# Optimization experiments

Measured on AMD Instinct MI355X. Metric: run time of the kernel, lower is better.

## Reference

```python
import jax, jax.numpy as jnp
import numpy as np

H_GRU = 32  # GRU hidden size fixed to 32 in the module


def setup_inputs() -> dict:
    key = jax.random.key(0)
    ks = jax.random.split(key, 12)
    B, C_in, H, W = 64, 64, 48, 160
    C_out = 64
    s_in = 1.0 / np.sqrt(C_in)
    s_h = 1.0 / np.sqrt(H_GRU)
    u = lambda k, shape: jax.random.uniform(k, shape, jnp.float32, -s_h, s_h)
    return {
        "x": jax.random.normal(ks[0], (B, C_in, H, W), jnp.float32),
        "conv_w": jax.random.normal(ks[1], (C_out, C_in), jnp.float32) * s_in,
        "conv_b": jax.random.normal(ks[2], (C_out,), jnp.float32) * s_in,
        "wih_f": u(ks[3], (3 * H_GRU, C_out)),
        "whh_f": u(ks[4], (3 * H_GRU, H_GRU)),
        "bih_f": u(ks[5], (3 * H_GRU,)),
        "bhh_f": u(ks[6], (3 * H_GRU,)),
        "wih_b": u(ks[7], (3 * H_GRU, C_out)),
        "whh_b": u(ks[8], (3 * H_GRU, H_GRU)),
        "bih_b": u(ks[9], (3 * H_GRU,)),
        "bhh_b": u(ks[10], (3 * H_GRU,)),
    }


def _gru_scan(pre, whh, bhh):
    # pre: [N, T, 3H] input-side gate pre-activations (already x@Wih^T + bih)
    N = pre.shape[0]

    def step(h, g):
        gh = h @ whh.T + bhh
        gi_r, gi_z, gi_n = jnp.split(g, 3, axis=-1)
        gh_r, gh_z, gh_n = jnp.split(gh, 3, axis=-1)
        r = jax.nn.sigmoid(gi_r + gh_r)
        z = jax.nn.sigmoid(gi_z + gh_z)
        n = jnp.tanh(gi_n + r * gh_n)
        h_new = (1.0 - z) * n + z * h
        return h_new, h_new

    h0 = jnp.zeros((N, H_GRU), pre.dtype)
    _, ys = jax.lax.scan(step, h0, jnp.swapaxes(pre, 0, 1))  # ys: [T, N, H]
    return jnp.swapaxes(ys, 0, 1)  # [N, T, H]


def reference(x, conv_w, conv_b, wih_f, whh_f, bih_f, bhh_f,
              wih_b, whh_b, bih_b, bhh_b):
    B, C_in, H, W = x.shape
    # 1x1 conv fused with the NCHW->NHWC permute
    y = jnp.einsum('bchw,oc->bhwo', x, conv_w) + conv_b  # [B, H, W, C_out]
    C_out = y.shape[-1]
    seq = y.reshape(B * H, W, C_out)  # GRU batch = B*H, seq_len = W
    # forward direction
    pre_f = jnp.einsum('ntc,gc->ntg', seq, wih_f) + bih_f
    out_f = _gru_scan(pre_f, whh_f, bhh_f)
    # backward direction: scan reversed sequence, then flip output back
    seq_r = seq[:, ::-1, :]
    pre_b = jnp.einsum('ntc,gc->ntg', seq_r, wih_b) + bih_b
    out_b = _gru_scan(pre_b, whh_b, bhh_b)[:, ::-1, :]
    out = jnp.concatenate([out_f, out_b], axis=-1)  # [B*H, W, 2*H_GRU]
    out = out.reshape(B, H, W, 2 * H_GRU)
    return jnp.transpose(out, (0, 3, 1, 2))  # back to NCHW
```

## Files before the change

kernel.cpp:

```cpp
#include <hip/hip_runtime.h>


typedef _Float16 f16x8 __attribute__((ext_vector_type(8)));
typedef _Float16 f16x4 __attribute__((ext_vector_type(4)));
typedef __fp16   pk16  __attribute__((ext_vector_type(2)));
typedef float    f32x4 __attribute__((ext_vector_type(4)));

#define HWSTRIDE 7680
#define NW 20
#define WS_WHH2_OFF 24576
#define WS_BIAS_OFF 36864

__global__ void fold_weights(const float* __restrict__ conv_w,
                             const float* __restrict__ conv_b,
                             const float* __restrict__ wih_f,
                             const float* __restrict__ bih_f,
                             const float* __restrict__ bhh_f,
                             const float* __restrict__ wih_b,
                             const float* __restrict__ bih_b,
                             const float* __restrict__ bhh_b,
                             const float* __restrict__ whh_f,
                             const float* __restrict__ whh_b,
                             void* wsv)
{
    _Float16* W2   = (_Float16*)wsv;
    _Float16* whh2 = (_Float16*)((char*)wsv + WS_WHH2_OFF);
    float*    bias = (float*)((char*)wsv + WS_BIAS_OFF);
    const int idx = blockIdx.x * 256 + threadIdx.x;
    if (idx < 12288) {
        const int d = idx / 6144, r = idx % 6144, g = r / 64, c = r % 64;
        const float* wih = d ? wih_b : wih_f;
        float acc = 0.f;
        for (int o = 0; o < 64; ++o) acc += wih[g * 64 + o] * conv_w[o * 64 + c];
        W2[idx] = (_Float16)acc;
    } else if (idx < 18432) {
        const int e2 = idx - 12288;
        const int dd = e2 / 3072, rr = e2 % 3072, g = rr / 32, k = rr % 32;
        const int qq = k >> 3, ee = k & 7;
        const int jsrc = (ee < 4) ? (qq * 4 + ee) : (16 + qq * 4 + (ee - 4));
        const float* whh = dd ? whh_b : whh_f;
        whh2[e2] = (_Float16)whh[g * 32 + jsrc];
    } else if (idx < 18688) {
        const int e = idx - 18432;
        const int d = e >> 7, rr = e & 127, kind = rr >> 5, j = rr & 31;
        const float* wih = d ? wih_b : wih_f;
        const float* bih = d ? bih_b : bih_f;
        const float* bhh = d ? bhh_b : bhh_f;
        float v;
        if (kind == 0 || kind == 1) {
            const int g = j + kind * 32;
            float b2 = bih[g];
            for (int o = 0; o < 64; ++o) b2 += wih[g * 64 + o] * conv_b[o];
            v = b2 + bhh[g];
        } else if (kind == 2) {
            const int g = j + 64;
            float b2 = bih[g];
            for (int o = 0; o < 64; ++o) b2 += wih[g * 64 + o] * conv_b[o];
            v = b2;
        } else {
            v = bhh[j + 64];
        }
        bias[(d * 4 + kind) * 32 + j] = v;
    }
}

static __device__ __forceinline__ unsigned pkh(float a, float b) {
    pk16 p = __builtin_amdgcn_cvt_pkrtz(a, b);
    return __builtin_bit_cast(unsigned, p);
}

#define BAR() do { asm volatile("s_waitcnt lgkmcnt(0)" ::: "memory"); \
                   __builtin_amdgcn_s_barrier();                      \
                   asm volatile("" ::: "memory"); } while (0)

__global__ __launch_bounds__(128, 1)
void gru_fused8(const float* __restrict__ x,
                const void* __restrict__ wsv,
                float* __restrict__ out)
{
    __shared__ __align__(16) _Float16 xt[1024 * 8];
    __shared__ __align__(16) _Float16 spre[2 * 8 * 16 * 96];

    const int bid  = blockIdx.x;
    const int d    = bid / 192;
    const int g    = bid % 192;
    const int b    = g / 3;
    const int h0   = (g % 3) * 16;
    const int lane = threadIdx.x & 63;
    const int wave = threadIdx.x >> 6;
    const int sw   = bid & 1;
    const int q    = lane >> 4;
    const int s16  = lane & 15;

    const float* xb = x + (size_t)b * 64 * HWSTRIDE + (size_t)h0 * 160;

    if (wave != sw) {
        const _Float16* W2 = (const _Float16*)wsv + (size_t)d * 96 * 64;
        f16x8 W2A[6][2];
        #pragma unroll
        for (int gt = 0; gt < 6; ++gt)
            #pragma unroll
            for (int kt = 0; kt < 2; ++kt)
                W2A[gt][kt] = *(const f16x8*)&W2[(gt * 16 + s16) * 64 + kt * 32 + q * 8];
        const float* bias = (const float*)((const char*)wsv + WS_BIAS_OFF) + d * 128;
        float biasC[6][4];
        #pragma unroll
        for (int gt = 0; gt < 6; ++gt)
            #pragma unroll
            for (int r = 0; r < 4; ++r)
                biasC[gt][r] = bias[(gt >> 1) * 32 + (gt & 1) * 16 + 4 * q + r];

        float4 pf[32];
        auto load_win = [&](int wi) {
            const int w0 = d ? (152 - 8 * wi) : (8 * wi);
            #pragma unroll
            for (int k = 0; k < 16; ++k) {
                const int row = lane + 64 * k;
                const float* p = xb + (size_t)(row >> 4) * HWSTRIDE + (row & 15) * 160 + w0;
                pf[2 * k]     = *(const float4*)p;
                pf[2 * k + 1] = *(const float4*)(p + 4);
            }
        };
        auto write_xt = [&]() {
            #pragma unroll
            for (int k = 0; k < 16; ++k) {
                const int row = lane + 64 * k;
                uint4 v;
                v.x = pkh(pf[2*k].x,   pf[2*k].y);
                v.y = pkh(pf[2*k].z,   pf[2*k].w);
                v.z = pkh(pf[2*k+1].x, pf[2*k+1].y);
                v.w = pkh(pf[2*k+1].z, pf[2*k+1].w);
                *(uint4*)&xt[row * 8] = v;
            }
        };
        auto project = [&](int wi) {
            _Float16* sp = &spre[(wi & 1) * 12288];
            for (int tt = 0; tt < 8; ++tt) {
                const int wl = d ? (7 - tt) : tt;
                const int base0 = (q * 8) * 128 + s16 * 8 + wl;
                f16x8 B0, B1;
                #pragma unroll
                for (int e = 0; e < 8; ++e) {
                    B0[e] = xt[base0 + e * 128];
                    B1[e] = xt[base0 + e * 128 + 4096];
                }
                #pragma unroll
                for (int gt = 0; gt < 6; ++gt) {
                    f32x4 acc = {biasC[gt][0], biasC[gt][1], biasC[gt][2], biasC[gt][3]};
                    acc = __builtin_amdgcn_mfma_f32_16x16x32_f16(W2A[gt][0], B0, acc, 0, 0, 0);
                    acc = __builtin_amdgcn_mfma_f32_16x16x32_f16(W2A[gt][1], B1, acc, 0, 0, 0);
                    uint2 v; v.x = pkh(acc[0], acc[1]); v.y = pkh(acc[2], acc[3]);
                    const int col = (gt * 16 + 4 * q) ^ ((s16 & 7) << 2);
                    *(uint2*)&sp[(tt * 16 + s16) * 96 + col] = v;
                }
            }
        };

        load_win(0);
        #pragma unroll 1
        for (int i = 0; i < NW; ++i) {
            write_xt();
            project(i);
            if (i + 1 < NW) load_win(i + 1);
            BAR();
        }
    } else {
        const _Float16* whh2 = (const _Float16*)((const char*)wsv + WS_WHH2_OFF)
                               + (size_t)d * 96 * 32;
        f16x8 whhA[6];
        #pragma unroll
        for (int gt = 0; gt < 6; ++gt)
            whhA[gt] = *(const f16x8*)&whh2[(gt * 16 + s16) * 32 + q * 8];
        const float* bias = (const float*)((const char*)wsv + WS_BIAS_OFF) + d * 128;
        float bhN[2][4];
        #pragma unroll
        for (int jh = 0; jh < 2; ++jh)
            #pragma unroll
            for (int r = 0; r < 4; ++r)
                bhN[jh][r] = bias[96 + jh * 16 + 4 * q + r];

        float* ob = out + ((size_t)b * 64 + d * 32) * HWSTRIDE + (size_t)(h0 + s16) * 160;
        f16x8 hB = {};
        f16x8 hB8[8];
        float hprev[8];
        #pragma unroll
        for (int uu = 0; uu < 8; ++uu) hprev[uu] = 0.f;

        int spcol[6];
        #pragma unroll
        for (int gt = 0; gt < 6; ++gt)
            spcol[gt] = (gt * 16 + 4 * q) ^ ((s16 & 7) << 2);

        #pragma unroll 1
        for (int i = 0; i < NW; ++i) {
            BAR();
            const _Float16* sp = &spre[(i & 1) * 12288];
            f16x4 pg[4][6];
            #pragma unroll
            for (int tt = 0; tt < 8; ++tt) {
                if ((tt & 3) == 0) {
                    #pragma unroll
                    for (int t4 = 0; t4 < 4; ++t4)
                        #pragma unroll
                        for (int gt = 0; gt < 6; ++gt)
                            pg[t4][gt] = *(const f16x4*)
                                &sp[((tt + t4) * 16 + s16) * 96 + spcol[gt]];
                }
                const f16x4 p0 = pg[tt & 3][0], p1 = pg[tt & 3][1];
                const f16x4 p2 = pg[tt & 3][2], p3 = pg[tt & 3][3];
                const f16x4 p4 = pg[tt & 3][4], p5 = pg[tt & 3][5];
                f32x4 aR0 = {(float)p0[0], (float)p0[1], (float)p0[2], (float)p0[3]};
                f32x4 aR1 = {(float)p1[0], (float)p1[1], (float)p1[2], (float)p1[3]};
                f32x4 aZ0 = {(float)p2[0], (float)p2[1], (float)p2[2], (float)p2[3]};
                f32x4 aZ1 = {(float)p3[0], (float)p3[1], (float)p3[2], (float)p3[3]};
                f32x4 aN0 = {bhN[0][0], bhN[0][1], bhN[0][2], bhN[0][3]};
                f32x4 aN1 = {bhN[1][0], bhN[1][1], bhN[1][2], bhN[1][3]};
                aR0 = __builtin_amdgcn_mfma_f32_16x16x32_f16(whhA[0], hB, aR0, 0, 0, 0);
                aR1 = __builtin_amdgcn_mfma_f32_16x16x32_f16(whhA[1], hB, aR1, 0, 0, 0);
                aZ0 = __builtin_amdgcn_mfma_f32_16x16x32_f16(whhA[2], hB, aZ0, 0, 0, 0);
                aZ1 = __builtin_amdgcn_mfma_f32_16x16x32_f16(whhA[3], hB, aZ1, 0, 0, 0);
                aN0 = __builtin_amdgcn_mfma_f32_16x16x32_f16(whhA[4], hB, aN0, 0, 0, 0);
                aN1 = __builtin_amdgcn_mfma_f32_16x16x32_f16(whhA[5], hB, aN1, 0, 0, 0);
                float hn[8];
                #pragma unroll
                for (int r = 0; r < 4; ++r) {
                    const float rr = __builtin_amdgcn_rcpf(1.f + __expf(-aR0[r]));
                    const float zz = __builtin_amdgcn_rcpf(1.f + __expf(-aZ0[r]));
                    float ta = fmaf(rr, aN0[r], (float)p4[r]);
                    ta = fminf(fmaxf(ta, -15.f), 15.f);
                    const float e2 = __expf(2.f * ta);
                    const float nn = (e2 - 1.f) * __builtin_amdgcn_rcpf(e2 + 1.f);
                    hn[r] = (1.f - zz) * nn + zz * hprev[r];
                }
                #pragma unroll
                for (int r = 0; r < 4; ++r) {
                    const float rr = __builtin_amdgcn_rcpf(1.f + __expf(-aR1[r]));
                    const float zz = __builtin_amdgcn_rcpf(1.f + __expf(-aZ1[r]));
                    float ta = fmaf(rr, aN1[r], (float)p5[r]);
                    ta = fminf(fmaxf(ta, -15.f), 15.f);
                    const float e2 = __expf(2.f * ta);
                    const float nn = (e2 - 1.f) * __builtin_amdgcn_rcpf(e2 + 1.f);
                    hn[4 + r] = (1.f - zz) * nn + zz * hprev[4 + r];
                }
                {
                    uint4 hu;
                    hu.x = pkh(hn[0], hn[1]); hu.y = pkh(hn[2], hn[3]);
                    hu.z = pkh(hn[4], hn[5]); hu.w = pkh(hn[6], hn[7]);
                    hB = __builtin_bit_cast(f16x8, hu);
                }
                hB8[tt] = hB;
                #pragma unroll
                for (int uu = 0; uu < 8; ++uu) hprev[uu] = hn[uu];
            }
            {
                const int w0 = d ? (152 - 8 * i) : (8 * i);
                #pragma unroll
                for (int e = 0; e < 8; ++e) {
                    const int j = (e >> 2) * 16 + 4 * q + (e & 3);
                    float* pw = ob + (size_t)j * HWSTRIDE + w0;
                    if (d == 0) {
                        *(float4*)(pw) = make_float4((float)hB8[0][e], (float)hB8[1][e],
                                                     (float)hB8[2][e], (float)hB8[3][e]);
                        *(float4*)(pw + 4) = make_float4((float)hB8[4][e], (float)hB8[5][e],
                                                         (float)hB8[6][e], (float)hB8[7][e]);
                    } else {
                        *(float4*)(pw) = make_float4((float)hB8[7][e], (float)hB8[6][e],
                                                     (float)hB8[5][e], (float)hB8[4][e]);
                        *(float4*)(pw + 4) = make_float4((float)hB8[3][e], (float)hB8[2][e],
                                                         (float)hB8[1][e], (float)hB8[0][e]);
                    }
                }
            }
        }
    }
}

extern "C" void kernel_launch(void* const* d_in, const int* in_sizes, int n_in,
                              void* d_out, int out_size, void* d_ws, size_t ws_size,
                              hipStream_t stream) {
    (void)in_sizes; (void)n_in; (void)ws_size; (void)out_size;
    fold_weights<<<dim3(74), dim3(256), 0, stream>>>(
        (const float*)d_in[1],
        (const float*)d_in[2],
        (const float*)d_in[3],
        (const float*)d_in[5],
        (const float*)d_in[6],
        (const float*)d_in[7],
        (const float*)d_in[9],
        (const float*)d_in[10],
        (const float*)d_in[4],
        (const float*)d_in[8],
        d_ws);
    gru_fused8<<<dim3(384), dim3(128), 0, stream>>>(
        (const float*)d_in[0],
        d_ws,
        (float*)d_out);
}
```

Measured before the change: 183.0 us.

## Split input transpose into separate kernel and fuse projection into single-wave GRU

Adds a pre-pass kernel that converts x to fp16 and transposes it into a workspace buffer laid out per (slice, timestep). The GRU kernel becomes a single 64-thread wave that computes the input projection with MFMA on each step, streaming inputs straight from global memory with a four-step register prefetch. This removes the producer/consumer wave split, the LDS staging and the per-window barriers. The cost is an extra full read and write of x through global memory, and it puts the projection MFMAs on the serial recurrence path. The old fused kernel is kept as a fallback when the workspace is too small.

```diff
diff --git a/kernel.cpp b/kernel.cpp
--- a/kernel.cpp
+++ b/kernel.cpp
@@ -7,9 +7,10 @@
 typedef float    f32x4 __attribute__((ext_vector_type(4)));
 
 #define HWSTRIDE 7680
-#define NW 20
 #define WS_WHH2_OFF 24576
 #define WS_BIAS_OFF 36864
+#define WS_X16_OFF  65536
+#define NWIN 20
 
 __global__ void fold_weights(const float* __restrict__ conv_w,
                              const float* __restrict__ conv_b,
@@ -69,6 +70,204 @@
     return __builtin_bit_cast(unsigned, p);
 }
 
+__global__ __launch_bounds__(256, 2)
+void xpose(const float* __restrict__ x, _Float16* __restrict__ x16)
+{
+    __shared__ _Float16 tile[16 * 16 * 64];
+    const int bid = blockIdx.x;
+    const int wc  = bid % 10;
+    const int hg  = (bid / 10) % 3;
+    const int b   = bid / 30;
+    const int t   = threadIdx.x;
+    const int s   = t >> 4;
+    const int c2  = t & 15;
+    const float* xb = x + (size_t)b * 64 * HWSTRIDE + (size_t)(hg * 16) * 160 + wc * 16;
+
+    float4 pf[4][4];
+    #pragma unroll
+    for (int cc = 0; cc < 4; ++cc)
+        #pragma unroll
+        for (int k = 0; k < 4; ++k)
+            pf[cc][k] = *(const float4*)(xb + (size_t)(c2 * 4 + cc) * HWSTRIDE
+                                         + (size_t)s * 160 + k * 4);
+    #pragma unroll
+    for (int k = 0; k < 4; ++k)
+        #pragma unroll
+        for (int m = 0; m < 4; ++m) {
+            const int w = k * 4 + m;
+            uint2 v;
+            v.x = pkh(((const float*)&pf[0][k])[m], ((const float*)&pf[1][k])[m]);
+            v.y = pkh(((const float*)&pf[2][k])[m], ((const float*)&pf[3][k])[m]);
+            const int baddr = (s * 2048 + w * 128 + c2 * 8) ^ ((s & 7) << 4);
+            *(uint2*)((char*)tile + baddr) = v;
+        }
+    __syncthreads();
+    #pragma unroll
+    for (int k = 0; k < 4; ++k) {
+        const int w  = k * 4 + (t >> 6);
+        const int ss = (t & 63) >> 2;
+        const int c0 = (t & 3) * 16;
+        uint2 dv[4];
+        #pragma unroll
+        for (int j = 0; j < 4; ++j) {
+            const int baddr = (ss * 2048 + w * 128 + c0 * 2 + j * 8) ^ ((ss & 7) << 4);
+            dv[j] = *(const uint2*)((char*)tile + baddr);
+        }
+        _Float16* op = x16 + ((size_t)(b * 3 + hg) * 160 + wc * 16 + w) * 1024 + ss * 64 + c0;
+        *(uint4*)(op)     = make_uint4(dv[0].x, dv[0].y, dv[1].x, dv[1].y);
+        *(uint4*)(op + 8) = make_uint4(dv[2].x, dv[2].y, dv[3].x, dv[3].y);
+    }
+}
+
+__global__ __launch_bounds__(64, 1)
+void gru_fused9(const _Float16* __restrict__ x16,
+                const void* __restrict__ wsv,
+                float* __restrict__ out)
+{
+    const int bid   = blockIdx.x;
+    const int d     = bid & 1;
+    const int slice = bid >> 1;
+    const int b     = slice / 3;
+    const int hg    = slice % 3;
+    const int h0    = hg * 16;
+    const int lane  = threadIdx.x;
+    const int q     = lane >> 4;
+    const int s16   = lane & 15;
+
+    const _Float16* W2 = (const _Float16*)wsv + (size_t)d * 96 * 64;
+    f16x8 W2A[6][2];
+    #pragma unroll
+    for (int gt = 0; gt < 6; ++gt)
+        #pragma unroll
+        for (int kt = 0; kt < 2; ++kt)
+            W2A[gt][kt] = *(const f16x8*)&W2[(gt * 16 + s16) * 64 + kt * 32 + q * 8];
+    const _Float16* whh2 = (const _Float16*)((const char*)wsv + WS_WHH2_OFF)
+                           + (size_t)d * 96 * 32;
+    f16x8 whhA[6];
+    #pragma unroll
+    for (int gt = 0; gt < 6; ++gt)
+        whhA[gt] = *(const f16x8*)&whh2[(gt * 16 + s16) * 32 + q * 8];
+    const float* bias = (const float*)((const char*)wsv + WS_BIAS_OFF) + d * 128;
+    float biasC[6][4];
+    #pragma unroll
+    for (int gt = 0; gt < 6; ++gt)
+        #pragma unroll
+        for (int r = 0; r < 4; ++r)
+            biasC[gt][r] = bias[(gt >> 1) * 32 + (gt & 1) * 16 + 4 * q + r];
+    float bhN[2][4];
+    #pragma unroll
+    for (int jh = 0; jh < 2; ++jh)
+        #pragma unroll
+        for (int r = 0; r < 4; ++r)
+            bhN[jh][r] = bias[96 + jh * 16 + 4 * q + r];
+
+    const _Float16* xsl = x16 + (size_t)slice * 160 * 1024 + s16 * 64 + q * 8;
+    float* ob = out + ((size_t)b * 64 + d * 32) * HWSTRIDE + (size_t)(h0 + s16) * 160;
+
+    f16x8 B0r[4], B1r[4];
+    auto loadB = [&](int s, f16x8& B0d, f16x8& B1d) {
+        const _Float16* p = xsl + (size_t)(d ? (159 - s) : s) * 1024;
+        B0d = *(const f16x8*)(p);
+        B1d = *(const f16x8*)(p + 32);
+    };
+    #pragma unroll
+    for (int s0 = 0; s0 < 4; ++s0) loadB(s0, B0r[s0], B1r[s0]);
+
+    f16x8 hB = {};
+    f16x8 hB8[8];
+    float hprev[8];
+    #pragma unroll
+    for (int uu = 0; uu < 8; ++uu) hprev[uu] = 0.f;
+
+    #pragma unroll 1
+    for (int i = 0; i < NWIN; ++i) {
+        #pragma unroll
+        for (int tt = 0; tt < 8; ++tt) {
+            const int s = i * 8 + tt;
+            f32x4 aR0 = {biasC[0][0], biasC[0][1], biasC[0][2], biasC[0][3]};
+            f32x4 aR1 = {biasC[1][0], biasC[1][1], biasC[1][2], biasC[1][3]};
+            f32x4 aZ0 = {biasC[2][0], biasC[2][1], biasC[2][2], biasC[2][3]};
+            f32x4 aZ1 = {biasC[3][0], biasC[3][1], biasC[3][2], biasC[3][3]};
+            f32x4 pN0 = {biasC[4][0], biasC[4][1], biasC[4][2], biasC[4][3]};
+            f32x4 pN1 = {biasC[5][0], biasC[5][1], biasC[5][2], biasC[5][3]};
+            f32x4 hN0 = {bhN[0][0], bhN[0][1], bhN[0][2], bhN[0][3]};
+            f32x4 hN1 = {bhN[1][0], bhN[1][1], bhN[1][2], bhN[1][3]};
+            aR0 = __builtin_amdgcn_mfma_f32_16x16x32_f16(W2A[0][0], B0r[tt & 3], aR0, 0, 0, 0);
+            aR0 = __builtin_amdgcn_mfma_f32_16x16x32_f16(W2A[0][1], B1r[tt & 3], aR0, 0, 0, 0);
+            aR1 = __builtin_amdgcn_mfma_f32_16x16x32_f16(W2A[1][0], B0r[tt & 3], aR1, 0, 0, 0);
+            aR1 = __builtin_amdgcn_mfma_f32_16x16x32_f16(W2A[1][1], B1r[tt & 3], aR1, 0, 0, 0);
+            aZ0 = __builtin_amdgcn_mfma_f32_16x16x32_f16(W2A[2][0], B0r[tt & 3], aZ0, 0, 0, 0);
+            aZ0 = __builtin_amdgcn_mfma_f32_16x16x32_f16(W2A[2][1], B1r[tt & 3], aZ0, 0, 0, 0);
+            aZ1 = __builtin_amdgcn_mfma_f32_16x16x32_f16(W2A[3][0], B0r[tt & 3], aZ1, 0, 0, 0);
+            aZ1 = __builtin_amdgcn_mfma_f32_16x16x32_f16(W2A[3][1], B1r[tt & 3], aZ1, 0, 0, 0);
+            pN0 = __builtin_amdgcn_mfma_f32_16x16x32_f16(W2A[4][0], B0r[tt & 3], pN0, 0, 0, 0);
+            pN0 = __builtin_amdgcn_mfma_f32_16x16x32_f16(W2A[4][1], B1r[tt & 3], pN0, 0, 0, 0);
+            pN1 = __builtin_amdgcn_mfma_f32_16x16x32_f16(W2A[5][0], B0r[tt & 3], pN1, 0, 0, 0);
+            pN1 = __builtin_amdgcn_mfma_f32_16x16x32_f16(W2A[5][1], B1r[tt & 3], pN1, 0, 0, 0);
+            aR0 = __builtin_amdgcn_mfma_f32_16x16x32_f16(whhA[0], hB, aR0, 0, 0, 0);
+            aR1 = __builtin_amdgcn_mfma_f32_16x16x32_f16(whhA[1], hB, aR1, 0, 0, 0);
+            aZ0 = __builtin_amdgcn_mfma_f32_16x16x32_f16(whhA[2], hB, aZ0, 0, 0, 0);
+            aZ1 = __builtin_amdgcn_mfma_f32_16x16x32_f16(whhA[3], hB, aZ1, 0, 0, 0);
+            hN0 = __builtin_amdgcn_mfma_f32_16x16x32_f16(whhA[4], hB, hN0, 0, 0, 0);
+            hN1 = __builtin_amdgcn_mfma_f32_16x16x32_f16(whhA[5], hB, hN1, 0, 0, 0);
+            if (tt < 4) {
+                loadB(s + 4, B0r[tt & 3], B1r[tt & 3]);
+            } else if (i + 1 < NWIN) {
+                loadB(s + 4, B0r[tt & 3], B1r[tt & 3]);
+            }
+            float hn[8];
+            #pragma unroll
+            for (int r = 0; r < 4; ++r) {
+                const float rr = __builtin_amdgcn_rcpf(1.f + __expf(-aR0[r]));
+                const float zz = __builtin_amdgcn_rcpf(1.f + __expf(-aZ0[r]));
+                float ta = fmaf(rr, hN0[r], pN0[r]);
+                ta = fminf(fmaxf(ta, -15.f), 15.f);
+                const float e2 = __expf(2.f * ta);
+                const float nn = (e2 - 1.f) * __builtin_amdgcn_rcpf(e2 + 1.f);
+                hn[r] = (1.f - zz) * nn + zz * hprev[r];
+            }
+            #pragma unroll
+            for (int r = 0; r < 4; ++r) {
+                const float rr = __builtin_amdgcn_rcpf(1.f + __expf(-aR1[r]));
+                const float zz = __builtin_amdgcn_rcpf(1.f + __expf(-aZ1[r]));
+                float ta = fmaf(rr, hN1[r], pN1[r]);
+                ta = fminf(fmaxf(ta, -15.f), 15.f);
+                const float e2 = __expf(2.f * ta);
+                const float nn = (e2 - 1.f) * __builtin_amdgcn_rcpf(e2 + 1.f);
+                hn[4 + r] = (1.f - zz) * nn + zz * hprev[4 + r];
+            }
+            {
+                uint4 hu;
+                hu.x = pkh(hn[0], hn[1]); hu.y = pkh(hn[2], hn[3]);
+                hu.z = pkh(hn[4], hn[5]); hu.w = pkh(hn[6], hn[7]);
+                hB = __builtin_bit_cast(f16x8, hu);
+            }
+            hB8[tt] = hB;
+            #pragma unroll
+            for (int uu = 0; uu < 8; ++uu) hprev[uu] = hn[uu];
+        }
+        {
+            const int w0 = d ? (152 - 8 * i) : (8 * i);
+            #pragma unroll
+            for (int e = 0; e < 8; ++e) {
+                const int j = (e >> 2) * 16 + 4 * q + (e & 3);
+                float* pw = ob + (size_t)j * HWSTRIDE + w0;
+                if (d == 0) {
+                    *(float4*)(pw)     = make_float4((float)hB8[0][e], (float)hB8[1][e],
+                                                     (float)hB8[2][e], (float)hB8[3][e]);
+                    *(float4*)(pw + 4) = make_float4((float)hB8[4][e], (float)hB8[5][e],
+                                                     (float)hB8[6][e], (float)hB8[7][e]);
+                } else {
+                    *(float4*)(pw)     = make_float4((float)hB8[7][e], (float)hB8[6][e],
+                                                     (float)hB8[5][e], (float)hB8[4][e]);
+                    *(float4*)(pw + 4) = make_float4((float)hB8[3][e], (float)hB8[2][e],
+                                                     (float)hB8[1][e], (float)hB8[0][e]);
+                }
+            }
+        }
+    }
+}
+
 #define BAR() do { asm volatile("s_waitcnt lgkmcnt(0)" ::: "memory"); \
                    __builtin_amdgcn_s_barrier();                      \
                    asm volatile("" ::: "memory"); } while (0)
@@ -158,10 +357,10 @@
 
         load_win(0);
         #pragma unroll 1
-        for (int i = 0; i < NW; ++i) {
+        for (int i = 0; i < NWIN; ++i) {
             write_xt();
             project(i);
-            if (i + 1 < NW) load_win(i + 1);
+            if (i + 1 < NWIN) load_win(i + 1);
             BAR();
         }
     } else {
@@ -192,7 +391,7 @@
             spcol[gt] = (gt * 16 + 4 * q) ^ ((s16 & 7) << 2);
 
         #pragma unroll 1
-        for (int i = 0; i < NW; ++i) {
+        for (int i = 0; i < NWIN; ++i) {
             BAR();
             const _Float16* sp = &spre[(i & 1) * 12288];
             f16x4 pg[4][6];
@@ -278,7 +477,7 @@
 extern "C" void kernel_launch(void* const* d_in, const int* in_sizes, int n_in,
                               void* d_out, int out_size, void* d_ws, size_t ws_size,
                               hipStream_t stream) {
-    (void)in_sizes; (void)n_in; (void)ws_size; (void)out_size;
+    (void)in_sizes; (void)n_in; (void)out_size;
     fold_weights<<<dim3(74), dim3(256), 0, stream>>>(
         (const float*)d_in[1],
         (const float*)d_in[2],
@@ -291,8 +490,13 @@
         (const float*)d_in[4],
         (const float*)d_in[8],
         d_ws);
-    gru_fused8<<<dim3(384), dim3(128), 0, stream>>>(
-        (const float*)d_in[0],
-        d_ws,
-        (float*)d_out);
+    const size_t need = (size_t)WS_X16_OFF + (size_t)192 * 160 * 1024 * 2;
+    if (ws_size >= need) {
+        _Float16* x16 = (_Float16*)((char*)d_ws + WS_X16_OFF);
+        xpose<<<dim3(1920), dim3(256), 0, stream>>>((const float*)d_in[0], x16);
+        gru_fused9<<<dim3(384), dim3(64), 0, stream>>>(x16, d_ws, (float*)d_out);
+    } else {
+        gru_fused8<<<dim3(384), dim3(128), 0, stream>>>(
+            (const float*)d_in[0], d_ws, (float*)d_out);
+    }
 }
```

New measurement: 204.6 us. 11.8% more time.
